# Kernel tuning notes

Hardware: AMD Instinct MI355X
Metric: run time of the kernel (lower is better)

## Reference

```python
import jax, jax.numpy as jnp
import numpy as np

EMB_DIM = 1024
N_HEADS = 16
HEAD_DIM = EMB_DIM // N_HEADS
MAX_SEQ_LEN = 2048
THETA = 10000.0
B, T = 2, 2048


def _precompute_rope(head_dim, max_seq_len, theta=THETA):
    freqs = 1.0 / theta ** (np.arange(0, head_dim, 2, dtype=np.float32) / head_dim)
    t = np.arange(max_seq_len, dtype=np.float32)
    ang = np.outer(t, freqs)  # [T, D/2]
    return jnp.asarray(np.cos(ang)), jnp.asarray(np.sin(ang))


def setup_inputs() -> dict:
    key = jax.random.key(0)
    kx, kqkv, kp, kb = jax.random.split(key, 4)
    x = jax.random.normal(kx, (B, T, EMB_DIM), dtype=jnp.float32)
    # nn.Linear weights stored as [out, in]; we keep [in, out] for x @ W
    s1 = 1.0 / np.sqrt(EMB_DIM)
    Wqkv = jax.random.uniform(kqkv, (EMB_DIM, 3 * EMB_DIM), minval=-s1, maxval=s1, dtype=jnp.float32)
    Wproj = jax.random.uniform(kp, (EMB_DIM, EMB_DIM), minval=-s1, maxval=s1, dtype=jnp.float32)
    bproj = jax.random.uniform(kb, (EMB_DIM,), minval=-s1, maxval=s1, dtype=jnp.float32)
    cos, sin = _precompute_rope(HEAD_DIM, MAX_SEQ_LEN)
    return {"x": x, "Wqkv": Wqkv, "Wproj": Wproj, "bproj": bproj, "cos": cos, "sin": sin}


def _apply_rope(x, cos, sin):
    # x: [B,H,T,D]; cos/sin: [max_T, D/2]
    T_ = x.shape[-2]
    c, s = cos[:T_], sin[:T_]  # [T, D/2], broadcasts over B,H
    xe, xo = x[..., ::2], x[..., 1::2]
    re = xe * c - xo * s
    ro = xe * s + xo * c
    return jnp.stack([re, ro], axis=-1).reshape(x.shape)


def reference(x, Wqkv, Wproj, bproj, cos, sin):
    Bq, Tq, C = x.shape
    qkv = x @ Wqkv  # [B,T,3C]
    q, k, v = jnp.split(qkv, 3, axis=-1)
    def to_heads(t):
        return t.reshape(Bq, Tq, N_HEADS, HEAD_DIM).transpose(0, 2, 1, 3)  # [B,H,T,D]
    q, k, v = to_heads(q), to_heads(k), to_heads(v)
    q = _apply_rope(q, cos, sin)
    k = _apply_rope(k, cos, sin)
    scale = 1.0 / jnp.sqrt(jnp.asarray(HEAD_DIM, dtype=x.dtype))
    scores = jnp.einsum('bhqd,bhkd->bhqk', q, k) * scale  # [B,H,T,T]
    causal = jnp.tril(jnp.ones((Tq, Tq), dtype=bool))
    scores = jnp.where(causal, scores, jnp.asarray(-jnp.inf, dtype=scores.dtype))
    attn = jax.nn.softmax(scores, axis=-1)
    out = jnp.einsum('bhqk,bhkd->bhqd', attn, v)  # [B,H,T,D]
    out = out.transpose(0, 2, 1, 3).reshape(Bq, Tq, C)
    return out @ Wproj + bproj
```

## Files before the change

kernel.cpp:

```cpp
#include <hip/hip_runtime.h>

typedef __attribute__((ext_vector_type(8))) short short8;
typedef __attribute__((ext_vector_type(4))) float f32x4;
typedef __attribute__((ext_vector_type(4))) unsigned short u16x4;
typedef __attribute__((ext_vector_type(8))) unsigned short u16x8;
typedef unsigned short ushort_t;

#define GLOAD16(gp, sp) __builtin_amdgcn_global_load_lds( \
    (const __attribute__((address_space(1))) void*)(gp),  \
    (__attribute__((address_space(3))) void*)(sp), 16, 0, 0)

#define MFMA(a, b, c) __builtin_amdgcn_mfma_f32_16x16x32_bf16(a, b, c, 0, 0, 0)

__device__ __forceinline__ ushort_t f2b(float f) {
    union { float f; unsigned u; } c; c.f = f;
    unsigned r = (c.u + 0x7FFFu + ((c.u >> 16) & 1u)) >> 16;
    return (ushort_t)r;
}
__device__ __forceinline__ float b2f(ushort_t u) {
    union { unsigned u; float f; } c; c.u = ((unsigned)u) << 16;
    return c.f;
}
__device__ __forceinline__ short8 packv(u16x4 a, u16x4 b) {
    u16x8 c = __builtin_shufflevector(a, b, 0, 1, 2, 3, 4, 5, 6, 7);
    union { u16x8 u; short8 s; } w; w.u = c; return w.s;
}

__global__ void cvt_bf16(const float* __restrict__ in, ushort_t* __restrict__ out, int n) {
    int i = (blockIdx.x * 256 + threadIdx.x) * 4;
    if (i < n) {
        f32x4 v = *(const f32x4*)(in + i);
        u16x4 o;
        #pragma unroll
        for (int j = 0; j < 4; j++) o[j] = f2b(v[j]);
        *(u16x4*)(out + i) = o;
    }
}

__global__ __launch_bounds__(256) void transpose_cvt(const float* __restrict__ in,
                                                     ushort_t* __restrict__ out,
                                                     int R, int Cc) {
    __shared__ float tile[32][33];
    int tx = threadIdx.x & 31, ty = threadIdx.x >> 5;
    int c0 = blockIdx.x * 32, r0 = blockIdx.y * 32;
    #pragma unroll
    for (int i = 0; i < 32; i += 8)
        tile[ty + i][tx] = in[(size_t)(r0 + ty + i) * Cc + c0 + tx];
    __syncthreads();
    #pragma unroll
    for (int i = 0; i < 32; i += 8)
        out[(size_t)(c0 + ty + i) * R + r0 + tx] = f2b(tile[tx][ty + i]);
}

template <bool F32OUT, bool BIAS>
__global__ __launch_bounds__(256) void gemm_bt(const ushort_t* __restrict__ A,
                                               const ushort_t* __restrict__ Bt,
                                               void* __restrict__ Cout,
                                               const float* __restrict__ bias,
                                               int M, int N, int K) {
    __shared__ ushort_t lA[128 * 32];
    __shared__ ushort_t lB[128 * 32];
    const int tid = threadIdx.x;
    const int l = tid & 63, wv = tid >> 6;
    const int g = l >> 4, q16 = l & 15;
    const int m0 = blockIdx.y * 128, n0 = blockIdx.x * 128;
    const int wr = wv >> 1, wc = wv & 1;

    f32x4 acc[4][4];
    #pragma unroll
    for (int i = 0; i < 4; i++)
        #pragma unroll
        for (int j = 0; j < 4; j++) acc[i][j] = (f32x4){0.f, 0.f, 0.f, 0.f};

    const ushort_t* ga = A + (size_t)(m0 + wv * 32 + (l >> 2)) * K + (l & 3) * 8;
    const ushort_t* gb = Bt + (size_t)(n0 + wv * 32 + (l >> 2)) * K + (l & 3) * 8;
    ushort_t* sa = lA + wv * 32 * 32;
    ushort_t* sb = lB + wv * 32 * 32;

    for (int k0 = 0; k0 < K; k0 += 32) {
        __syncthreads();
        GLOAD16(ga + k0, sa);
        GLOAD16(ga + k0 + (size_t)16 * K, sa + 16 * 32);
        GLOAD16(gb + k0, sb);
        GLOAD16(gb + k0 + (size_t)16 * K, sb + 16 * 32);
        __syncthreads();

        short8 af[4], bf[4];
        #pragma unroll
        for (int mi = 0; mi < 4; mi++)
            af[mi] = *(const short8*)(lA + (wr * 64 + mi * 16 + q16) * 32 + g * 8);
        #pragma unroll
        for (int ni = 0; ni < 4; ni++)
            bf[ni] = *(const short8*)(lB + (wc * 64 + ni * 16 + q16) * 32 + g * 8);
        #pragma unroll
        for (int mi = 0; mi < 4; mi++)
            #pragma unroll
            for (int ni = 0; ni < 4; ni++)
                acc[mi][ni] = MFMA(af[mi], bf[ni], acc[mi][ni]);
    }

    #pragma unroll
    for (int ni = 0; ni < 4; ni++) {
        const int n = n0 + wc * 64 + ni * 16 + q16;
        float bv = 0.f;
        if (BIAS) bv = bias[n];
        #pragma unroll
        for (int mi = 0; mi < 4; mi++) {
            const int mbase = m0 + wr * 64 + mi * 16 + g * 4;
            #pragma unroll
            for (int r = 0; r < 4; r++) {
                if (F32OUT) {
                    ((float*)Cout)[(size_t)(mbase + r) * N + n] = acc[mi][ni][r] + bv;
                } else {
                    ((ushort_t*)Cout)[(size_t)(mbase + r) * N + n] = f2b(acc[mi][ni][r]);
                }
            }
        }
    }
}

__global__ void rope_scatter(const ushort_t* __restrict__ qkv,
                             const float* __restrict__ cosT, const float* __restrict__ sinT,
                             ushort_t* __restrict__ Qr, ushort_t* __restrict__ Kr,
                             ushort_t* __restrict__ Vt) {
    const float QS = 0.1803368801f;
    int tid = blockIdx.x * 256 + threadIdx.x;
    {
        int dc = tid & 7;
        int bht = tid >> 3;
        int t = bht & 2047, bh = bht >> 11;
        int b = bh >> 4, h = bh & 15;
        size_t mrow = ((size_t)b * 2048 + t) * 3072;
        short8 qv = *(const short8*)(qkv + mrow + h * 64 + dc * 8);
        short8 kv = *(const short8*)(qkv + mrow + 1024 + h * 64 + dc * 8);
        f32x4 cv = *(const f32x4*)(cosT + t * 32 + dc * 4);
        f32x4 sv = *(const f32x4*)(sinT + t * 32 + dc * 4);
        short8 qo, ko;
        #pragma unroll
        for (int j = 0; j < 4; j++) {
            float qe = b2f((ushort_t)qv[2 * j]), qod = b2f((ushort_t)qv[2 * j + 1]);
            float ke = b2f((ushort_t)kv[2 * j]), kod = b2f((ushort_t)kv[2 * j + 1]);
            qo[2 * j]     = (short)f2b((qe * cv[j] - qod * sv[j]) * QS);
            qo[2 * j + 1] = (short)f2b((qe * sv[j] + qod * cv[j]) * QS);
            ko[2 * j]     = (short)f2b(ke * cv[j] - kod * sv[j]);
            ko[2 * j + 1] = (short)f2b(ke * sv[j] + kod * cv[j]);
        }
        *(short8*)(Qr + ((size_t)bh * 2048 + t) * 64 + dc * 8) = qo;
        *(short8*)(Kr + ((size_t)bh * 2048 + t) * 64 + dc * 8) = ko;
    }
    {
        int t = tid & 2047;
        int rest = tid >> 11;
        int dc = rest & 7, bh = rest >> 3;
        int b = bh >> 4, h = bh & 15;
        const ushort_t* vs = qkv + ((size_t)b * 2048 + t) * 3072 + 2048 + h * 64 + dc * 8;
        #pragma unroll
        for (int j = 0; j < 8; j++)
            Vt[((size_t)bh * 64 + dc * 8 + j) * 2048 + t] = vs[j];
    }
}


#define TILE(S0, S1, QPOS, MSK, LS, O0, O1, O2, O3, PV0, PV1, PV2, PV3, kvb_) do { \
    float sv_[8];                                                              \
    sv_[0] = S0[0]; sv_[1] = S0[1]; sv_[2] = S0[2]; sv_[3] = S0[3];            \
    sv_[4] = S1[0]; sv_[5] = S1[1]; sv_[6] = S1[2]; sv_[7] = S1[3];            \
    if (MSK) {                                                                 \
        int kb0_ = (kvb_) + (g << 2);                                          \
        _Pragma("unroll") for (int r_ = 0; r_ < 4; r_++) {                     \
            if (kb0_ + r_ > (QPOS))      sv_[r_]     = -INFINITY;              \
            if (kb0_ + 16 + r_ > (QPOS)) sv_[4 + r_] = -INFINITY;              \
        }                                                                      \
    }                                                                          \
    float pp_[8];                                                              \
    _Pragma("unroll") for (int i_ = 0; i_ < 8; i_++)                           \
        pp_[i_] = __builtin_amdgcn_exp2f(sv_[i_]);                             \
    LS += ((pp_[0] + pp_[1]) + (pp_[2] + pp_[3])) +                            \
          ((pp_[4] + pp_[5]) + (pp_[6] + pp_[7]));                             \
    union { short8 s; unsigned u[4]; } pu_;                                    \
    asm("v_cvt_pk_bf16_f32 %0, %1, %2" : "=v"(pu_.u[0]) : "v"(pp_[0]), "v"(pp_[1])); \
    asm("v_cvt_pk_bf16_f32 %0, %1, %2" : "=v"(pu_.u[1]) : "v"(pp_[2]), "v"(pp_[3])); \
    asm("v_cvt_pk_bf16_f32 %0, %1, %2" : "=v"(pu_.u[2]) : "v"(pp_[4]), "v"(pp_[5])); \
    asm("v_cvt_pk_bf16_f32 %0, %1, %2" : "=v"(pu_.u[3]) : "v"(pp_[6]), "v"(pp_[7])); \
    O0 = MFMA(PV0, pu_.s, O0);                                                 \
    O1 = MFMA(PV1, pu_.s, O1);                                                 \
    O2 = MFMA(PV2, pu_.s, O2);                                                 \
    O3 = MFMA(PV3, pu_.s, O3);                                                 \
} while (0)

#define EPI(LS, O0, O1, O2, O3, QPOS) do {                                     \
    float l2_ = LS + __shfl_xor(LS, 16);                                       \
    l2_ += __shfl_xor(l2_, 32);                                                \
    float ri_ = 1.0f / l2_;                                                    \
    ushort_t* op_ = Aout + ((size_t)(bq * 2048 + (QPOS)) << 10) + (h << 6) + (g << 2); \
    u16x4 o_;                                                                  \
    o_[0] = f2b(O0[0] * ri_); o_[1] = f2b(O0[1] * ri_);                        \
    o_[2] = f2b(O0[2] * ri_); o_[3] = f2b(O0[3] * ri_);                        \
    *(u16x4*)op_ = o_;                                                         \
    o_[0] = f2b(O1[0] * ri_); o_[1] = f2b(O1[1] * ri_);                        \
    o_[2] = f2b(O1[2] * ri_); o_[3] = f2b(O1[3] * ri_);                        \
    *(u16x4*)(op_ + 16) = o_;                                                  \
    o_[0] = f2b(O2[0] * ri_); o_[1] = f2b(O2[1] * ri_);                        \
    o_[2] = f2b(O2[2] * ri_); o_[3] = f2b(O2[3] * ri_);                        \
    *(u16x4*)(op_ + 32) = o_;                                                  \
    o_[0] = f2b(O3[0] * ri_); o_[1] = f2b(O3[1] * ri_);                        \
    o_[2] = f2b(O3[2] * ri_); o_[3] = f2b(O3[3] * ri_);                        \
    *(u16x4*)(op_ + 48) = o_;                                                  \
} while (0)

__global__ __launch_bounds__(256) void attn_fwd(const ushort_t* __restrict__ Qr,
                                                const ushort_t* __restrict__ Kr,
                                                const ushort_t* __restrict__ Vt,
                                                ushort_t* __restrict__ Aout) {
    __shared__ ushort_t Ksh[2][2048];
    __shared__ ushort_t Vsh[2][2048];

    const int tid = threadIdx.x;
    const int l = tid & 63, wv = tid >> 6;
    const int g = l >> 4, q16 = l & 15;
    const int xcd = blockIdx.x & 7, loc = blockIdx.x >> 3;
    const int bh = (xcd << 2) | (loc >> 4);
    const int slot = loc & 15;
    const int p = slot + (wv << 4);
    const int qlo = p << 4, qhi = (127 - p) << 4;
    const int qpos_l = qlo + q16, qpos_h = qhi + q16;
    const int bq = bh >> 4, h = bh & 15;

    const int ntot_w  = (qhi + 47) >> 5;
    const int nlo_w   = (qlo + 47) >> 5;
    const int ntot_bk = (((127 - slot) << 4) + 47) >> 5;

    const ushort_t* Qp = Qr + ((size_t)bh * 2048) * 64;
    short8 ql0 = *(const short8*)(Qp + (size_t)qpos_l * 64 + g * 8);
    short8 ql1 = *(const short8*)(Qp + (size_t)qpos_l * 64 + g * 8 + 32);
    short8 qh0 = *(const short8*)(Qp + (size_t)qpos_h * 64 + g * 8);
    short8 qh1 = *(const short8*)(Qp + (size_t)qpos_h * 64 + g * 8 + 32);

    const ushort_t* Kb = Kr + (size_t)bh * 2048 * 64;
    const ushort_t* Vb = Vt + (size_t)bh * 64 * 2048;

    const ushort_t* ksrc = Kb + (size_t)(wv * 8 + (l >> 3)) * 64 + (((l & 7) ^ (l >> 3)) << 3);
    const ushort_t* vsrc = Vb + (size_t)(wv * 16 + (l >> 2)) * 2048 + (((l & 3) ^ ((l >> 2) & 3)) << 3);
    ushort_t* kdst0 = &Ksh[0][wv * 512]; ushort_t* kdst1 = &Ksh[1][wv * 512];
    ushort_t* vdst0 = &Vsh[0][wv * 512]; ushort_t* vdst1 = &Vsh[1][wv * 512];

#define STAGE(b_, t_) do {                                                     \
    GLOAD16(ksrc + (size_t)(t_) * 2048, (b_) ? kdst1 : kdst0);                 \
    GLOAD16(vsrc + (t_) * 32,           (b_) ? vdst1 : vdst0);                 \
} while (0)

    const int kx = (q16 & 7) << 4;
    const int kb_lo0 = q16 * 128 + ((g * 16) ^ kx);
    const int kb_hi0 = q16 * 128 + ((64 + g * 16) ^ kx);
    const int kb_lo1 = kb_lo0 + 16 * 128;
    const int kb_hi1 = kb_hi0 + 16 * 128;
    const int vx = (q16 & 3) << 4;
    const int vb0 = ((g * 8) ^ vx);
    const int vb1 = ((g * 8 + 32) ^ vx);

    float ls_l = 0.f, ls_h = 0.f;
    f32x4 ol0 = {0.f,0.f,0.f,0.f}, ol1 = {0.f,0.f,0.f,0.f};
    f32x4 ol2 = {0.f,0.f,0.f,0.f}, ol3 = {0.f,0.f,0.f,0.f};
    f32x4 oh0 = {0.f,0.f,0.f,0.f}, oh1 = {0.f,0.f,0.f,0.f};
    f32x4 oh2 = {0.f,0.f,0.f,0.f}, oh3 = {0.f,0.f,0.f,0.f};

    STAGE(0, 0);
    __syncthreads();

    for (int t = 0; t < ntot_bk; ++t) {
        const int nxt = t + 1;
        if (nxt < ntot_bk) {
            if (nxt & 1) STAGE(1, nxt); else STAGE(0, nxt);
        }
        const int kvb = t << 5;
        if (t < ntot_w) {
            const char* Kc = (const char*)(t & 1 ? Ksh[1] : Ksh[0]);
            const char* Vc = (const char*)(t & 1 ? Vsh[1] : Vsh[0]);
            short8 k0lo = *(const short8*)(Kc + kb_lo0);
            short8 k0hi = *(const short8*)(Kc + kb_hi0);
            short8 k1lo = *(const short8*)(Kc + kb_lo1);
            short8 k1hi = *(const short8*)(Kc + kb_hi1);
            f32x4 h0 = {0.f,0.f,0.f,0.f}, h1 = {0.f,0.f,0.f,0.f};
            f32x4 l0 = {0.f,0.f,0.f,0.f}, l1 = {0.f,0.f,0.f,0.f};
            const bool lo_on = t < nlo_w;
            h0 = MFMA(k0lo, qh0, h0);
            h0 = MFMA(k0hi, qh1, h0);
            h1 = MFMA(k1lo, qh0, h1);
            h1 = MFMA(k1hi, qh1, h1);
            if (lo_on) {
                l0 = MFMA(k0lo, ql0, l0);
                l0 = MFMA(k0hi, ql1, l0);
                l1 = MFMA(k1lo, ql0, l1);
                l1 = MFMA(k1hi, ql1, l1);
            }
            short8 pv0, pv1, pv2, pv3;
            {
                const char* vr0 = Vc + (q16) * 64;
                pv0 = packv(*(const u16x4*)(vr0 + vb0), *(const u16x4*)(vr0 + vb1));
                const char* vr1 = vr0 + 16 * 64;
                pv1 = packv(*(const u16x4*)(vr1 + vb0), *(const u16x4*)(vr1 + vb1));
                const char* vr2 = vr1 + 16 * 64;
                pv2 = packv(*(const u16x4*)(vr2 + vb0), *(const u16x4*)(vr2 + vb1));
                const char* vr3 = vr2 + 16 * 64;
                pv3 = packv(*(const u16x4*)(vr3 + vb0), *(const u16x4*)(vr3 + vb1));
            }
            TILE(h0, h1, qpos_h, kvb + 31 > qhi, ls_h,
                 oh0, oh1, oh2, oh3, pv0, pv1, pv2, pv3, kvb);
            if (lo_on)
                TILE(l0, l1, qpos_l, kvb + 31 > qlo, ls_l,
                     ol0, ol1, ol2, ol3, pv0, pv1, pv2, pv3, kvb);
        }
        __syncthreads();
    }

    EPI(ls_l, ol0, ol1, ol2, ol3, qpos_l);
    EPI(ls_h, oh0, oh1, oh2, oh3, qpos_h);
#undef STAGE
}

extern "C" void kernel_launch(void* const* d_in, const int* in_sizes, int n_in,
                              void* d_out, int out_size, void* d_ws, size_t ws_size,
                              hipStream_t stream) {
    const float* x     = (const float*)d_in[0];
    const float* Wqkv  = (const float*)d_in[1];
    const float* Wproj = (const float*)d_in[2];
    const float* bproj = (const float*)d_in[3];
    const float* cosT  = (const float*)d_in[4];
    const float* sinT  = (const float*)d_in[5];

    char* ws = (char*)d_ws;
    ushort_t* xb     = (ushort_t*)(ws);
    ushort_t* WqkvT  = (ushort_t*)(ws + (8u  << 20));
    ushort_t* WprojT = (ushort_t*)(ws + (14u << 20));
    ushort_t* qkv    = (ushort_t*)(ws + (16u << 20));
    ushort_t* Qr     = (ushort_t*)(ws + (40u << 20));
    ushort_t* Kr     = (ushort_t*)(ws + (48u << 20));
    ushort_t* Vt     = (ushort_t*)(ws + (56u << 20));
    ushort_t* aout   = (ushort_t*)(ws + (64u << 20));

    cvt_bf16<<<4096, 256, 0, stream>>>(x, xb, 4096 * 1024);
    transpose_cvt<<<dim3(96, 32), 256, 0, stream>>>(Wqkv, WqkvT, 1024, 3072);
    transpose_cvt<<<dim3(32, 32), 256, 0, stream>>>(Wproj, WprojT, 1024, 1024);

    gemm_bt<false, false><<<dim3(24, 32), 256, 0, stream>>>(xb, WqkvT, (void*)qkv, nullptr,
                                                            4096, 3072, 1024);
    rope_scatter<<<2048, 256, 0, stream>>>(qkv, cosT, sinT, Qr, Kr, Vt);
    attn_fwd<<<512, 256, 0, stream>>>(Qr, Kr, Vt, aout);
    gemm_bt<true, true><<<dim3(8, 32), 256, 0, stream>>>(aout, WprojT, d_out, bproj,
                                                         4096, 1024, 1024);
}
```

Before: 208.0 us.

## Double attention KV tile to 64 keys with permuted V layout for 16B loads

Increases the attention inner-loop KV tile from 32 to 64 keys, halving the number of loop iterations and __syncthreads barriers. V is stored with its sequence positions permuted so each lane can read a contiguous 16-byte short8 instead of packing two 8-byte loads. Query row assignment across waves is interleaved, and slot order is reversed for half the heads to balance causal work. Shared memory doubles and register pressure rises; launch bounds now request two blocks per CU.

```diff
diff --git a/kernel.cpp b/kernel.cpp
--- a/kernel.cpp
+++ b/kernel.cpp
@@ -3,7 +3,6 @@
 typedef __attribute__((ext_vector_type(8))) short short8;
 typedef __attribute__((ext_vector_type(4))) float f32x4;
 typedef __attribute__((ext_vector_type(4))) unsigned short u16x4;
-typedef __attribute__((ext_vector_type(8))) unsigned short u16x8;
 typedef unsigned short ushort_t;
 
 #define GLOAD16(gp, sp) __builtin_amdgcn_global_load_lds( \
@@ -20,10 +19,6 @@
 __device__ __forceinline__ float b2f(ushort_t u) {
     union { unsigned u; float f; } c; c.u = ((unsigned)u) << 16;
     return c.f;
-}
-__device__ __forceinline__ short8 packv(u16x4 a, u16x4 b) {
-    u16x8 c = __builtin_shufflevector(a, b, 0, 1, 2, 3, 4, 5, 6, 7);
-    union { u16x8 u; short8 s; } w; w.u = c; return w.s;
 }
 
 __global__ void cvt_bf16(const float* __restrict__ in, ushort_t* __restrict__ out, int n) {
@@ -154,39 +149,52 @@
         int dc = rest & 7, bh = rest >> 3;
         int b = bh >> 4, h = bh & 15;
         const ushort_t* vs = qkv + ((size_t)b * 2048 + t) * 3072 + 2048 + h * 64 + dc * 8;
+        int tp = (t & ~31) + ((t & 12) << 1) + ((t & 16) >> 2) + (t & 3);
         #pragma unroll
         for (int j = 0; j < 8; j++)
-            Vt[((size_t)bh * 64 + dc * 8 + j) * 2048 + t] = vs[j];
-    }
-}
-
-
-#define TILE(S0, S1, QPOS, MSK, LS, O0, O1, O2, O3, PV0, PV1, PV2, PV3, kvb_) do { \
-    float sv_[8];                                                              \
-    sv_[0] = S0[0]; sv_[1] = S0[1]; sv_[2] = S0[2]; sv_[3] = S0[3];            \
-    sv_[4] = S1[0]; sv_[5] = S1[1]; sv_[6] = S1[2]; sv_[7] = S1[3];            \
-    if (MSK) {                                                                 \
-        int kb0_ = (kvb_) + (g << 2);                                          \
-        _Pragma("unroll") for (int r_ = 0; r_ < 4; r_++) {                     \
-            if (kb0_ + r_ > (QPOS))      sv_[r_]     = -INFINITY;              \
-            if (kb0_ + 16 + r_ > (QPOS)) sv_[4 + r_] = -INFINITY;              \
-        }                                                                      \
-    }                                                                          \
-    float pp_[8];                                                              \
-    _Pragma("unroll") for (int i_ = 0; i_ < 8; i_++)                           \
-        pp_[i_] = __builtin_amdgcn_exp2f(sv_[i_]);                             \
-    LS += ((pp_[0] + pp_[1]) + (pp_[2] + pp_[3])) +                            \
-          ((pp_[4] + pp_[5]) + (pp_[6] + pp_[7]));                             \
-    union { short8 s; unsigned u[4]; } pu_;                                    \
-    asm("v_cvt_pk_bf16_f32 %0, %1, %2" : "=v"(pu_.u[0]) : "v"(pp_[0]), "v"(pp_[1])); \
-    asm("v_cvt_pk_bf16_f32 %0, %1, %2" : "=v"(pu_.u[1]) : "v"(pp_[2]), "v"(pp_[3])); \
-    asm("v_cvt_pk_bf16_f32 %0, %1, %2" : "=v"(pu_.u[2]) : "v"(pp_[4]), "v"(pp_[5])); \
-    asm("v_cvt_pk_bf16_f32 %0, %1, %2" : "=v"(pu_.u[3]) : "v"(pp_[6]), "v"(pp_[7])); \
-    O0 = MFMA(PV0, pu_.s, O0);                                                 \
-    O1 = MFMA(PV1, pu_.s, O1);                                                 \
-    O2 = MFMA(PV2, pu_.s, O2);                                                 \
-    O3 = MFMA(PV3, pu_.s, O3);                                                 \
-} while (0)
+            Vt[((size_t)bh * 64 + dc * 8 + j) * 2048 + tp] = vs[j];
+    }
+}
+
+
+__device__ __forceinline__ void tile64(
+    const f32x4& S0, const f32x4& S1, const f32x4& S2, const f32x4& S3,
+    int qpos, bool msk, int kvb, int g, float& ls,
+    f32x4& o0, f32x4& o1, f32x4& o2, f32x4& o3,
+    const short8& va0, const short8& va1, const short8& va2, const short8& va3,
+    const short8& vb0, const short8& vb1, const short8& vb2, const short8& vb3) {
+    float sv[16];
+    #pragma unroll
+    for (int r = 0; r < 4; r++) {
+        sv[r] = S0[r]; sv[4 + r] = S1[r]; sv[8 + r] = S2[r]; sv[12 + r] = S3[r];
+    }
+    if (msk) {
+        int kb0 = kvb + (g << 2);
+        #pragma unroll
+        for (int G = 0; G < 4; G++)
+            #pragma unroll
+            for (int r = 0; r < 4; r++)
+                if (kb0 + 16 * G + r > qpos) sv[G * 4 + r] = -INFINITY;
+    }
+    float pp[16];
+    #pragma unroll
+    for (int i = 0; i < 16; i++) pp[i] = __builtin_amdgcn_exp2f(sv[i]);
+    ls += (((pp[0] + pp[1]) + (pp[2] + pp[3])) + ((pp[4] + pp[5]) + (pp[6] + pp[7]))) +
+          (((pp[8] + pp[9]) + (pp[10] + pp[11])) + ((pp[12] + pp[13]) + (pp[14] + pp[15])));
+    union { short8 s; unsigned u[4]; } p0, p1;
+    asm("v_cvt_pk_bf16_f32 %0, %1, %2" : "=v"(p0.u[0]) : "v"(pp[0]), "v"(pp[1]));
+    asm("v_cvt_pk_bf16_f32 %0, %1, %2" : "=v"(p0.u[1]) : "v"(pp[2]), "v"(pp[3]));
+    asm("v_cvt_pk_bf16_f32 %0, %1, %2" : "=v"(p0.u[2]) : "v"(pp[4]), "v"(pp[5]));
+    asm("v_cvt_pk_bf16_f32 %0, %1, %2" : "=v"(p0.u[3]) : "v"(pp[6]), "v"(pp[7]));
+    asm("v_cvt_pk_bf16_f32 %0, %1, %2" : "=v"(p1.u[0]) : "v"(pp[8]), "v"(pp[9]));
+    asm("v_cvt_pk_bf16_f32 %0, %1, %2" : "=v"(p1.u[1]) : "v"(pp[10]), "v"(pp[11]));
+    asm("v_cvt_pk_bf16_f32 %0, %1, %2" : "=v"(p1.u[2]) : "v"(pp[12]), "v"(pp[13]));
+    asm("v_cvt_pk_bf16_f32 %0, %1, %2" : "=v"(p1.u[3]) : "v"(pp[14]), "v"(pp[15]));
+    o0 = MFMA(va0, p0.s, o0); o0 = MFMA(vb0, p1.s, o0);
+    o1 = MFMA(va1, p0.s, o1); o1 = MFMA(vb1, p1.s, o1);
+    o2 = MFMA(va2, p0.s, o2); o2 = MFMA(vb2, p1.s, o2);
+    o3 = MFMA(va3, p0.s, o3); o3 = MFMA(vb3, p1.s, o3);
+}
 
 #define EPI(LS, O0, O1, O2, O3, QPOS) do {                                     \
     float l2_ = LS + __shfl_xor(LS, 16);                                       \
@@ -208,27 +216,29 @@
     *(u16x4*)(op_ + 48) = o_;                                                  \
 } while (0)
 
-__global__ __launch_bounds__(256) void attn_fwd(const ushort_t* __restrict__ Qr,
-                                                const ushort_t* __restrict__ Kr,
-                                                const ushort_t* __restrict__ Vt,
-                                                ushort_t* __restrict__ Aout) {
-    __shared__ ushort_t Ksh[2][2048];
-    __shared__ ushort_t Vsh[2][2048];
+__global__ __launch_bounds__(256, 2) void attn_fwd(const ushort_t* __restrict__ Qr,
+                                                   const ushort_t* __restrict__ Kr,
+                                                   const ushort_t* __restrict__ Vt,
+                                                   ushort_t* __restrict__ Aout) {
+    __shared__ __attribute__((aligned(16))) ushort_t Ksh[2][4096];
+    __shared__ __attribute__((aligned(16))) ushort_t Vsh[2][4096];
 
     const int tid = threadIdx.x;
     const int l = tid & 63, wv = tid >> 6;
     const int g = l >> 4, q16 = l & 15;
     const int xcd = blockIdx.x & 7, loc = blockIdx.x >> 3;
-    const int bh = (xcd << 2) | (loc >> 4);
-    const int slot = loc & 15;
-    const int p = slot + (wv << 4);
+    const int h2 = loc >> 4;
+    const int bh = (xcd << 2) | h2;
+    int slot = loc & 15;
+    if (h2 & 2) slot = 15 - slot;
+    const int p = slot * 4 + wv;
     const int qlo = p << 4, qhi = (127 - p) << 4;
     const int qpos_l = qlo + q16, qpos_h = qhi + q16;
     const int bq = bh >> 4, h = bh & 15;
 
-    const int ntot_w  = (qhi + 47) >> 5;
-    const int nlo_w   = (qlo + 47) >> 5;
-    const int ntot_bk = (((127 - slot) << 4) + 47) >> 5;
+    const int ntot_bk = (((127 - slot * 4) << 4) + 79) >> 6;
+    const int ntot_w  = (qhi + 79) >> 6;
+    const int nlo_w   = (qlo + 79) >> 6;
 
     const ushort_t* Qp = Qr + ((size_t)bh * 2048) * 64;
     short8 ql0 = *(const short8*)(Qp + (size_t)qpos_l * 64 + g * 8);
@@ -239,24 +249,24 @@
     const ushort_t* Kb = Kr + (size_t)bh * 2048 * 64;
     const ushort_t* Vb = Vt + (size_t)bh * 64 * 2048;
 
-    const ushort_t* ksrc = Kb + (size_t)(wv * 8 + (l >> 3)) * 64 + (((l & 7) ^ (l >> 3)) << 3);
-    const ushort_t* vsrc = Vb + (size_t)(wv * 16 + (l >> 2)) * 2048 + (((l & 3) ^ ((l >> 2) & 3)) << 3);
-    ushort_t* kdst0 = &Ksh[0][wv * 512]; ushort_t* kdst1 = &Ksh[1][wv * 512];
-    ushort_t* vdst0 = &Vsh[0][wv * 512]; ushort_t* vdst1 = &Vsh[1][wv * 512];
-
-#define STAGE(b_, t_) do {                                                     \
-    GLOAD16(ksrc + (size_t)(t_) * 2048, (b_) ? kdst1 : kdst0);                 \
-    GLOAD16(vsrc + (t_) * 32,           (b_) ? vdst1 : vdst0);                 \
+    const ushort_t* ksrcA = Kb + (size_t)(wv * 16 + (l >> 3)) * 64 + (((l & 7) ^ (l >> 3)) << 3);
+    const ushort_t* vsrcA = Vb + (size_t)(wv * 16 + (l >> 2)) * 2048 + (((l & 3) ^ ((l >> 3) & 3)) << 3);
+
+#define STAGE(buf_, t_) do {                                                   \
+    const ushort_t* ka_ = ksrcA + (size_t)(t_) * 4096;                         \
+    const ushort_t* va_ = vsrcA + (t_) * 64;                                   \
+    GLOAD16(ka_,       &Ksh[buf_][wv * 1024]);                                 \
+    GLOAD16(ka_ + 512, &Ksh[buf_][wv * 1024 + 512]);                           \
+    GLOAD16(va_,       &Vsh[buf_][wv * 512]);                                  \
+    GLOAD16(va_ + 32,  &Vsh[buf_][2048 + wv * 512]);                           \
 } while (0)
 
-    const int kx = (q16 & 7) << 4;
-    const int kb_lo0 = q16 * 128 + ((g * 16) ^ kx);
-    const int kb_hi0 = q16 * 128 + ((64 + g * 16) ^ kx);
-    const int kb_lo1 = kb_lo0 + 16 * 128;
-    const int kb_hi1 = kb_hi0 + 16 * 128;
-    const int vx = (q16 & 3) << 4;
-    const int vb0 = ((g * 8) ^ vx);
-    const int vb1 = ((g * 8 + 32) ^ vx);
+    const int kx  = q16 & 7;
+    const int kq  = q16 * 128;
+    const int kh0 = (g ^ kx) << 4;
+    const int kh1 = ((g + 4) ^ kx) << 4;
+    const int vsw = (g ^ ((q16 >> 1) & 3)) << 4;
+    const int vq  = q16 * 64;
 
     float ls_l = 0.f, ls_h = 0.f;
     f32x4 ol0 = {0.f,0.f,0.f,0.f}, ol1 = {0.f,0.f,0.f,0.f};
@@ -272,43 +282,46 @@
         if (nxt < ntot_bk) {
             if (nxt & 1) STAGE(1, nxt); else STAGE(0, nxt);
         }
-        const int kvb = t << 5;
         if (t < ntot_w) {
             const char* Kc = (const char*)(t & 1 ? Ksh[1] : Ksh[0]);
             const char* Vc = (const char*)(t & 1 ? Vsh[1] : Vsh[0]);
-            short8 k0lo = *(const short8*)(Kc + kb_lo0);
-            short8 k0hi = *(const short8*)(Kc + kb_hi0);
-            short8 k1lo = *(const short8*)(Kc + kb_lo1);
-            short8 k1hi = *(const short8*)(Kc + kb_hi1);
-            f32x4 h0 = {0.f,0.f,0.f,0.f}, h1 = {0.f,0.f,0.f,0.f};
-            f32x4 l0 = {0.f,0.f,0.f,0.f}, l1 = {0.f,0.f,0.f,0.f};
+            short8 k00 = *(const short8*)(Kc + kq + kh0);
+            short8 k01 = *(const short8*)(Kc + kq + kh1);
+            short8 k10 = *(const short8*)(Kc + kq + 2048 + kh0);
+            short8 k11 = *(const short8*)(Kc + kq + 2048 + kh1);
+            short8 k20 = *(const short8*)(Kc + kq + 4096 + kh0);
+            short8 k21 = *(const short8*)(Kc + kq + 4096 + kh1);
+            short8 k30 = *(const short8*)(Kc + kq + 6144 + kh0);
+            short8 k31 = *(const short8*)(Kc + kq + 6144 + kh1);
+            f32x4 s0 = {0.f,0.f,0.f,0.f}, s1 = {0.f,0.f,0.f,0.f};
+            f32x4 s2 = {0.f,0.f,0.f,0.f}, s3 = {0.f,0.f,0.f,0.f};
+            s0 = MFMA(k00, qh0, s0); s0 = MFMA(k01, qh1, s0);
+            s1 = MFMA(k10, qh0, s1); s1 = MFMA(k11, qh1, s1);
+            s2 = MFMA(k20, qh0, s2); s2 = MFMA(k21, qh1, s2);
+            s3 = MFMA(k30, qh0, s3); s3 = MFMA(k31, qh1, s3);
             const bool lo_on = t < nlo_w;
-            h0 = MFMA(k0lo, qh0, h0);
-            h0 = MFMA(k0hi, qh1, h0);
-            h1 = MFMA(k1lo, qh0, h1);
-            h1 = MFMA(k1hi, qh1, h1);
+            f32x4 u0 = {0.f,0.f,0.f,0.f}, u1 = {0.f,0.f,0.f,0.f};
+            f32x4 u2 = {0.f,0.f,0.f,0.f}, u3 = {0.f,0.f,0.f,0.f};
             if (lo_on) {
-                l0 = MFMA(k0lo, ql0, l0);
-                l0 = MFMA(k0hi, ql1, l0);
-                l1 = MFMA(k1lo, ql0, l1);
-                l1 = MFMA(k1hi, ql1, l1);
+                u0 = MFMA(k00, ql0, u0); u0 = MFMA(k01, ql1, u0);
+                u1 = MFMA(k10, ql0, u1); u1 = MFMA(k11, ql1, u1);
+                u2 = MFMA(k20, ql0, u2); u2 = MFMA(k21, ql1, u2);
+                u3 = MFMA(k30, ql0, u3); u3 = MFMA(k31, ql1, u3);
             }
-            short8 pv0, pv1, pv2, pv3;
-            {
-                const char* vr0 = Vc + (q16) * 64;
-                pv0 = packv(*(const u16x4*)(vr0 + vb0), *(const u16x4*)(vr0 + vb1));
-                const char* vr1 = vr0 + 16 * 64;
-                pv1 = packv(*(const u16x4*)(vr1 + vb0), *(const u16x4*)(vr1 + vb1));
-                const char* vr2 = vr1 + 16 * 64;
-                pv2 = packv(*(const u16x4*)(vr2 + vb0), *(const u16x4*)(vr2 + vb1));
-                const char* vr3 = vr2 + 16 * 64;
-                pv3 = packv(*(const u16x4*)(vr3 + vb0), *(const u16x4*)(vr3 + vb1));
-            }
-            TILE(h0, h1, qpos_h, kvb + 31 > qhi, ls_h,
-                 oh0, oh1, oh2, oh3, pv0, pv1, pv2, pv3, kvb);
+            short8 va0 = *(const short8*)(Vc + vq + vsw);
+            short8 va1 = *(const short8*)(Vc + vq + 1024 + vsw);
+            short8 va2 = *(const short8*)(Vc + vq + 2048 + vsw);
+            short8 va3 = *(const short8*)(Vc + vq + 3072 + vsw);
+            short8 vb0 = *(const short8*)(Vc + 4096 + vq + vsw);
+            short8 vb1 = *(const short8*)(Vc + 4096 + vq + 1024 + vsw);
+            short8 vb2 = *(const short8*)(Vc + 4096 + vq + 2048 + vsw);
+            short8 vb3 = *(const short8*)(Vc + 4096 + vq + 3072 + vsw);
+            const int kvb = t << 6;
+            tile64(s0, s1, s2, s3, qpos_h, kvb + 63 > qhi, kvb, g, ls_h,
+                   oh0, oh1, oh2, oh3, va0, va1, va2, va3, vb0, vb1, vb2, vb3);
             if (lo_on)
-                TILE(l0, l1, qpos_l, kvb + 31 > qlo, ls_l,
-                     ol0, ol1, ol2, ol3, pv0, pv1, pv2, pv3, kvb);
+                tile64(u0, u1, u2, u3, qpos_l, kvb + 63 > qlo, kvb, g, ls_l,
+                       ol0, ol1, ol2, ol3, va0, va1, va2, va3, vb0, vb1, vb2, vb3);
         }
         __syncthreads();
     }
```

Result: faster. 191.0 us (-8.2%).
